# Kernel optimization log

Hardware: AMD Instinct MI355X
Metric: run time of the kernel (lower is better)

The kernel has to match this reference:

```python
import jax, jax.numpy as jnp
import numpy as np
from functools import partial

SAMPLE_RATE = 44100
CUTOFF_HZ = 20.0
# one-pole high-pass coefficient: y[i] = x[i] - x[i-1] + alpha * y[i-1]
ALPHA = float(np.exp(-2.0 * np.pi * CUTOFF_HZ / SAMPLE_RATE))


def setup_inputs() -> dict:
    key = jax.random.key(0)
    k1, k2, k3, k4 = jax.random.split(key, 4)
    B, N = 64, 262144
    return {
        "x": jax.random.normal(k1, (B, N), dtype=jnp.float32),
        "drive": jax.random.uniform(k2, (B, 1), dtype=jnp.float32),
        "bias": jax.random.uniform(k3, (B, 1), dtype=jnp.float32),
        "mix": jax.random.uniform(k4, (B, 1), dtype=jnp.float32),
        "type_idx": 0,
    }


def _waveshape(processed, type_idx):
    if type_idx == 0:
        return jnp.tanh(processed)
    elif type_idx == 1:
        return jnp.clip(processed, -1.0, 1.0)
    elif type_idx == 2:
        return jnp.abs(jnp.remainder(processed + 1.0, 4.0) - 2.0) - 1.0
    elif type_idx == 3:
        return jnp.sin(processed * (np.pi / 2))
    else:
        return processed / (1.0 + jnp.abs(processed))


def _high_pass_filter(x):
    # x: [B, N]; sequential first-order IIR over the time axis via lax.scan
    B = x.shape[0]
    zeros = jnp.zeros((B,), dtype=x.dtype)

    def step(carry, xt):
        last_x, last_y = carry
        yt = xt - last_x + ALPHA * last_y
        return (xt, yt), yt

    _, yT = jax.lax.scan(step, (zeros, zeros), x.T)  # yT: [N, B]
    return yT.T


def reference(x, drive, bias, mix, type_idx):
    drive_gain = jnp.power(10.0, drive * 2.4)
    dc_offset = bias * 2.0 - 1.0
    processed = (x + dc_offset) * drive_gain
    distorted = _waveshape(processed, type_idx)
    distorted = _high_pass_filter(distorted)
    return (1.0 - mix) * x + mix * distorted
```

## Files before the change

kernel.cpp:

```cpp
#include <hip/hip_runtime.h>
#include <math.h>

#define TPB 1024
#define WAVES (TPB / 64)
#define PER_WAVE 1024
#define BLK (WAVES * PER_WAVE)
#define HALO 2048
#define CSZ (BLK - HALO)

typedef float v4f __attribute__((ext_vector_type(4)));

__device__ __forceinline__ float shape(float xs, int ty, float g, float dc,
                                       float c1, float c0) {
    if (ty == 0) {
        float e2 = __builtin_amdgcn_exp2f(fmaf(xs, c1, c0));
        return fmaf(-2.0f, __builtin_amdgcn_rcpf(e2 + 1.0f), 1.0f);
    }
    float p = (xs + dc) * g;
    if (ty == 1) {
        return fminf(fmaxf(p, -1.0f), 1.0f);
    } else if (ty == 2) {
        float r = p + 1.0f;
        float rem = r - 4.0f * floorf(r * 0.25f);
        return fabsf(rem - 2.0f) - 1.0f;
    } else if (ty == 3) {
        return __sinf(p * 1.5707963267948966f);
    } else {
        return p / (1.0f + fabsf(p));
    }
}

__global__ void __launch_bounds__(TPB, 8)
dist_kernel(const float* __restrict__ x,
            const float* __restrict__ drive,
            const float* __restrict__ bias,
            const float* __restrict__ mix,
            const int* __restrict__ type_idx,
            float* __restrict__ out,
            int N, float alpha, float beta)
{
    const int row  = blockIdx.y;
    const int tid  = threadIdx.x;
    const int lane = tid & 63;
    const int wv   = tid >> 6;
    const int ty   = *type_idx;

    const float g  = exp2f(drive[row] * 7.972672880099267f);
    const float dc = bias[row] * 2.0f - 1.0f;
    const float mm = mix[row];
    const float om = 1.0f - mm;
    const float c1 = g * 2.8853900817779268f;
    const float c0 = dc * c1;

    const long long rowBase = (long long)row * (long long)N;
    const float* __restrict__ xr = x + rowBase;
    float* __restrict__ outr = out + rowBase;

    const int outStart = (int)blockIdx.x * CSZ;
    const int wbase = outStart - HALO + wv * PER_WAVE;

    v4f d4[4];
    v4f mx4[4];
    #pragma unroll
    for (int k = 0; k < 4; ++k) {
        const int j = wbase + k * 256 + lane * 4;
        if (j >= 0 && j + 4 <= N) {
            v4f xv = *reinterpret_cast<const v4f*>(xr + j);
            mx4[k].x = om * xv.x; d4[k].x = shape(xv.x, ty, g, dc, c1, c0);
            mx4[k].y = om * xv.y; d4[k].y = shape(xv.y, ty, g, dc, c1, c0);
            mx4[k].z = om * xv.z; d4[k].z = shape(xv.z, ty, g, dc, c1, c0);
            mx4[k].w = om * xv.w; d4[k].w = shape(xv.w, ty, g, dc, c1, c0);
        } else {
            float xs; bool in;
            in = (j+0 >= 0) && (j+0 < N); xs = in ? xr[j+0] : 0.0f; mx4[k].x = om * xs; d4[k].x = in ? shape(xs, ty, g, dc, c1, c0) : 0.0f;
            in = (j+1 >= 0) && (j+1 < N); xs = in ? xr[j+1] : 0.0f; mx4[k].y = om * xs; d4[k].y = in ? shape(xs, ty, g, dc, c1, c0) : 0.0f;
            in = (j+2 >= 0) && (j+2 < N); xs = in ? xr[j+2] : 0.0f; mx4[k].z = om * xs; d4[k].z = in ? shape(xs, ty, g, dc, c1, c0) : 0.0f;
            in = (j+3 >= 0) && (j+3 < N); xs = in ? xr[j+3] : 0.0f; mx4[k].w = om * xs; d4[k].w = in ? shape(xs, ty, g, dc, c1, c0) : 0.0f;
        }
    }

    const float a2 = alpha * alpha;
    const float a4 = a2 * a2;
    float iv[4];
    #pragma unroll
    for (int k = 0; k < 4; ++k) {
        float acc = d4[k].x;
        acc = fmaf(alpha, acc, d4[k].y);
        acc = fmaf(alpha, acc, d4[k].z);
        acc = fmaf(alpha, acc, d4[k].w);
        iv[k] = acc;
    }

    float a256;
    #pragma unroll
    for (int k = 0; k < 4; ++k) {
        float v = iv[k];
        float m = a4;
        #pragma unroll
        for (int off = 1; off < 64; off <<= 1) {
            float up = __shfl_up(v, off, 64);
            if (lane >= off) v = fmaf(m, up, v);
            m *= m;
        }
        iv[k] = v;
        a256 = m;
    }

    float T[4];
    T[0] = __shfl(iv[0], 63, 64);
    T[1] = __shfl(iv[1], 63, 64);
    T[2] = __shfl(iv[2], 63, 64);
    T[3] = __shfl(iv[3], 63, 64);
    const float Twave = fmaf(a256, fmaf(a256, fmaf(a256, T[0], T[1]), T[2]), T[3]);
    const float a1024 = (a256 * a256) * (a256 * a256);

    __shared__ float wtot[WAVES];
    if (lane == 0) wtot[wv] = Twave;
    __syncthreads();
    float P = 0.0f;
    for (int w = 0; w < wv; ++w) P = fmaf(a1024, P, wtot[w]);

    float apl = 1.0f, b = a4;
    #pragma unroll
    for (int i = 0; i < 6; ++i) { if ((lane >> i) & 1) apl *= b; b *= b; }

    float S  = 0.0f;
    float aK = 1.0f;
    #pragma unroll
    for (int k = 0; k < 4; ++k) {
        const int j = wbase + k * 256 + lane * 4;
        const float Ck = fmaf(aK, P, S);
        float ex = __shfl_up(iv[k], 1, 64);
        if (lane == 0) ex = 0.0f;
        const float zin = fmaf(apl, Ck, ex);

        if (j >= outStart && j < N) {
            float z = zin;
            v4f ov;
            float y;
            y = fmaf(-beta, z, d4[k].x); ov.x = fmaf(mm, y, mx4[k].x); z = fmaf(alpha, z, d4[k].x);
            y = fmaf(-beta, z, d4[k].y); ov.y = fmaf(mm, y, mx4[k].y); z = fmaf(alpha, z, d4[k].y);
            y = fmaf(-beta, z, d4[k].z); ov.z = fmaf(mm, y, mx4[k].z); z = fmaf(alpha, z, d4[k].z);
            y = fmaf(-beta, z, d4[k].w); ov.w = fmaf(mm, y, mx4[k].w);
            if (j + 4 <= N) {
                __builtin_nontemporal_store(ov, reinterpret_cast<v4f*>(outr + j));
            } else {
                if (j + 0 < N) outr[j + 0] = ov.x;
                if (j + 1 < N) outr[j + 1] = ov.y;
                if (j + 2 < N) outr[j + 2] = ov.z;
                if (j + 3 < N) outr[j + 3] = ov.w;
            }
        }
        S  = fmaf(a256, S, T[k]);
        aK *= a256;
    }
}

extern "C" void kernel_launch(void* const* d_in, const int* in_sizes, int n_in,
                              void* d_out, int out_size, void* d_ws, size_t ws_size,
                              hipStream_t stream) {
    const float* x     = (const float*)d_in[0];
    const float* drive = (const float*)d_in[1];
    const float* bias  = (const float*)d_in[2];
    const float* mixp  = (const float*)d_in[3];
    const int*   tyi   = (const int*)d_in[4];
    float* out = (float*)d_out;

    const int B = in_sizes[1];
    const int N = in_sizes[0] / B;

    const double alpha_d = exp(-2.0 * M_PI * 20.0 / 44100.0);
    const float alpha = (float)alpha_d;
    const float beta  = (float)(1.0 - alpha_d);

    const int nChunks = (N + CSZ - 1) / CSZ;
    dim3 grid(nChunks, B);
    dist_kernel<<<grid, TPB, 0, stream>>>(x, drive, bias, mixp, tyi, out, N, alpha, beta);
}
```

Baseline: 128.8 us.

## Loop persistent blocks over chunks with carried IIR state and DPP scans

Each block now walks several consecutive chunks of a row, carrying the IIR state across chunks instead of recomputing a large halo per chunk; only one halo segment per block is computed. The intra-wave scan uses DPP row operations and readlane instead of shuffles, and the next chunk's input is prefetched while the current one is processed. This reduces redundant halo loads and compute, but shrinks the grid to few blocks per row, which lowers parallelism and memory-level concurrency.

```diff
diff --git a/kernel.cpp b/kernel.cpp
--- a/kernel.cpp
+++ b/kernel.cpp
@@ -1,14 +1,37 @@
 #include <hip/hip_runtime.h>
 #include <math.h>
 
-#define TPB 1024
+#define TPB 512
 #define WAVES (TPB / 64)
 #define PER_WAVE 1024
-#define BLK (WAVES * PER_WAVE)
+#define CHUNK (WAVES * PER_WAVE)
+#define NB 8
 #define HALO 2048
-#define CSZ (BLK - HALO)
 
 typedef float v4f __attribute__((ext_vector_type(4)));
+
+template<int CTRL, int RM, int BM, bool BC>
+__device__ __forceinline__ float dppf(float v) {
+    return __int_as_float(__builtin_amdgcn_update_dpp(
+        0, __float_as_int(v), CTRL, RM, BM, BC));
+}
+
+__device__ __forceinline__ float readlane_f(float v, int l) {
+    return __int_as_float(__builtin_amdgcn_readlane(__float_as_int(v), l));
+}
+
+__device__ __forceinline__ float scan_iir(float v, float mo1, float mo2,
+                                          float mo4, float mo8,
+                                          float w1, float w2) {
+    float b;
+    b = dppf<0x111, 0xF, 0xF, true >(v); v = fmaf(mo1, b, v);
+    b = dppf<0x112, 0xF, 0xF, true >(v); v = fmaf(mo2, b, v);
+    b = dppf<0x114, 0xF, 0xF, true >(v); v = fmaf(mo4, b, v);
+    b = dppf<0x118, 0xF, 0xF, true >(v); v = fmaf(mo8, b, v);
+    b = dppf<0x142, 0xA, 0xF, false>(v); v = fmaf(w1,  b, v);
+    b = dppf<0x143, 0xC, 0xF, false>(v); v = fmaf(w2,  b, v);
+    return v;
+}
 
 __device__ __forceinline__ float shape(float xs, int ty, float g, float dc,
                                        float c1, float c0) {
@@ -30,7 +53,23 @@
     }
 }
 
-__global__ void __launch_bounds__(TPB, 8)
+__device__ __forceinline__ void load_chunk(v4f xv[4], const float* __restrict__ xr,
+                                           int base, int N) {
+    #pragma unroll
+    for (int k = 0; k < 4; ++k) {
+        const int j = base + k * 256;
+        if (j + 4 <= N) {
+            xv[k] = *reinterpret_cast<const v4f*>(xr + j);
+        } else {
+            xv[k].x = (j + 0 < N) ? xr[j + 0] : 0.0f;
+            xv[k].y = (j + 1 < N) ? xr[j + 1] : 0.0f;
+            xv[k].z = (j + 2 < N) ? xr[j + 2] : 0.0f;
+            xv[k].w = (j + 3 < N) ? xr[j + 3] : 0.0f;
+        }
+    }
+}
+
+__global__ void __launch_bounds__(TPB, 4)
 dist_kernel(const float* __restrict__ x,
             const float* __restrict__ drive,
             const float* __restrict__ bias,
@@ -40,10 +79,18 @@
             int N, float alpha, float beta)
 {
     const int row  = blockIdx.y;
+    const int bx   = blockIdx.x;
     const int tid  = threadIdx.x;
     const int lane = tid & 63;
     const int wv   = tid >> 6;
     const int ty   = *type_idx;
+
+    const int nChunks = (N + CHUNK - 1) / CHUNK;
+    const int cpb = (nChunks + NB - 1) / NB;
+    const int cFirst = bx * cpb;
+    if (cFirst >= nChunks) return;
+    const int cLast = min(cFirst + cpb, nChunks);
+    const int spanStart = cFirst * CHUNK;
 
     const float g  = exp2f(drive[row] * 7.972672880099267f);
     const float dc = bias[row] * 2.0f - 1.0f;
@@ -56,92 +103,104 @@
     const float* __restrict__ xr = x + rowBase;
     float* __restrict__ outr = out + rowBase;
 
-    const int outStart = (int)blockIdx.x * CSZ;
-    const int wbase = outStart - HALO + wv * PER_WAVE;
-
-    v4f d4[4];
-    v4f mx4[4];
-    #pragma unroll
-    for (int k = 0; k < 4; ++k) {
-        const int j = wbase + k * 256 + lane * 4;
-        if (j >= 0 && j + 4 <= N) {
-            v4f xv = *reinterpret_cast<const v4f*>(xr + j);
-            mx4[k].x = om * xv.x; d4[k].x = shape(xv.x, ty, g, dc, c1, c0);
-            mx4[k].y = om * xv.y; d4[k].y = shape(xv.y, ty, g, dc, c1, c0);
-            mx4[k].z = om * xv.z; d4[k].z = shape(xv.z, ty, g, dc, c1, c0);
-            mx4[k].w = om * xv.w; d4[k].w = shape(xv.w, ty, g, dc, c1, c0);
-        } else {
-            float xs; bool in;
-            in = (j+0 >= 0) && (j+0 < N); xs = in ? xr[j+0] : 0.0f; mx4[k].x = om * xs; d4[k].x = in ? shape(xs, ty, g, dc, c1, c0) : 0.0f;
-            in = (j+1 >= 0) && (j+1 < N); xs = in ? xr[j+1] : 0.0f; mx4[k].y = om * xs; d4[k].y = in ? shape(xs, ty, g, dc, c1, c0) : 0.0f;
-            in = (j+2 >= 0) && (j+2 < N); xs = in ? xr[j+2] : 0.0f; mx4[k].z = om * xs; d4[k].z = in ? shape(xs, ty, g, dc, c1, c0) : 0.0f;
-            in = (j+3 >= 0) && (j+3 < N); xs = in ? xr[j+3] : 0.0f; mx4[k].w = om * xs; d4[k].w = in ? shape(xs, ty, g, dc, c1, c0) : 0.0f;
-        }
-    }
-
-    const float a2 = alpha * alpha;
-    const float a4 = a2 * a2;
-    float iv[4];
-    #pragma unroll
-    for (int k = 0; k < 4; ++k) {
-        float acc = d4[k].x;
-        acc = fmaf(alpha, acc, d4[k].y);
-        acc = fmaf(alpha, acc, d4[k].z);
-        acc = fmaf(alpha, acc, d4[k].w);
-        iv[k] = acc;
-    }
-
-    float a256;
-    #pragma unroll
-    for (int k = 0; k < 4; ++k) {
-        float v = iv[k];
-        float m = a4;
-        #pragma unroll
-        for (int off = 1; off < 64; off <<= 1) {
-            float up = __shfl_up(v, off, 64);
-            if (lane >= off) v = fmaf(m, up, v);
-            m *= m;
-        }
-        iv[k] = v;
-        a256 = m;
-    }
-
-    float T[4];
-    T[0] = __shfl(iv[0], 63, 64);
-    T[1] = __shfl(iv[1], 63, 64);
-    T[2] = __shfl(iv[2], 63, 64);
-    T[3] = __shfl(iv[3], 63, 64);
-    const float Twave = fmaf(a256, fmaf(a256, fmaf(a256, T[0], T[1]), T[2]), T[3]);
-    const float a1024 = (a256 * a256) * (a256 * a256);
-
-    __shared__ float wtot[WAVES];
-    if (lane == 0) wtot[wv] = Twave;
+    const float A2 = alpha * alpha;
+    const float A4 = A2 * A2;
+    const float A8 = A4 * A4;
+    const float A16 = A8 * A8;
+    const float A32 = A16 * A16;
+    const float A64 = A32 * A32;
+    const float A128 = A64 * A64;
+    const float A256 = A128 * A128;
+    const float A512 = A256 * A256;
+    const float A1024 = A512 * A512;
+    const float invA4 = 1.0f / A4;
+
+    float p15 = 1.0f;
+    {
+        float b = A4; const int n = lane & 15;
+        #pragma unroll
+        for (int i = 0; i < 4; ++i) { if ((n >> i) & 1) p15 *= b; b *= b; }
+    }
+    const float p31 = (lane & 16) ? p15 * A64  : p15;
+    const float apl = (lane & 32) ? p31 * A128 : p31;
+    const float w1 = A4 * p15;
+    const float w2 = A4 * p31;
+
+    __shared__ float wtot[2][WAVES];
+    const int wvOff = wv * PER_WAVE + lane * 4;
+
+    v4f xc[4];
+    load_chunk(xc, xr, spanStart + wvOff, N);
+
+    float carry = 0.0f;
+    if (bx > 0) {
+        const int j = spanStart - HALO + wv * 256 + lane * 4;
+        const v4f hx = *reinterpret_cast<const v4f*>(xr + j);
+        float r = shape(hx.x, ty, g, dc, c1, c0);
+        r = fmaf(alpha, r, shape(hx.y, ty, g, dc, c1, c0));
+        r = fmaf(alpha, r, shape(hx.z, ty, g, dc, c1, c0));
+        r = fmaf(alpha, r, shape(hx.w, ty, g, dc, c1, c0));
+        const float s = scan_iir(r, A4, A8, A16, A32, w1, w2);
+        if (lane == 63) wtot[1][wv] = s;
+    }
     __syncthreads();
-    float P = 0.0f;
-    for (int w = 0; w < wv; ++w) P = fmaf(a1024, P, wtot[w]);
-
-    float apl = 1.0f, b = a4;
-    #pragma unroll
-    for (int i = 0; i < 6; ++i) { if ((lane >> i) & 1) apl *= b; b *= b; }
-
-    float S  = 0.0f;
-    float aK = 1.0f;
-    #pragma unroll
-    for (int k = 0; k < 4; ++k) {
-        const int j = wbase + k * 256 + lane * 4;
-        const float Ck = fmaf(aK, P, S);
-        float ex = __shfl_up(iv[k], 1, 64);
-        if (lane == 0) ex = 0.0f;
-        const float zin = fmaf(apl, Ck, ex);
-
-        if (j >= outStart && j < N) {
-            float z = zin;
-            v4f ov;
-            float y;
-            y = fmaf(-beta, z, d4[k].x); ov.x = fmaf(mm, y, mx4[k].x); z = fmaf(alpha, z, d4[k].x);
-            y = fmaf(-beta, z, d4[k].y); ov.y = fmaf(mm, y, mx4[k].y); z = fmaf(alpha, z, d4[k].y);
-            y = fmaf(-beta, z, d4[k].z); ov.z = fmaf(mm, y, mx4[k].z); z = fmaf(alpha, z, d4[k].z);
-            y = fmaf(-beta, z, d4[k].w); ov.w = fmaf(mm, y, mx4[k].w);
+    if (bx > 0) {
+        #pragma unroll
+        for (int w = 0; w < WAVES; ++w) carry = fmaf(A256, carry, wtot[1][w]);
+    }
+
+    int par = 0;
+    for (int c = cFirst; c < cLast; ++c, par ^= 1) {
+        const int cb = c * CHUNK;
+        const bool more = (c + 1 < cLast);
+        v4f xn[4];
+        if (more) load_chunk(xn, xr, cb + CHUNK + wvOff, N);
+
+        v4f d4[4];
+        #pragma unroll
+        for (int k = 0; k < 4; ++k) {
+            d4[k].x = shape(xc[k].x, ty, g, dc, c1, c0);
+            d4[k].y = shape(xc[k].y, ty, g, dc, c1, c0);
+            d4[k].z = shape(xc[k].z, ty, g, dc, c1, c0);
+            d4[k].w = shape(xc[k].w, ty, g, dc, c1, c0);
+        }
+
+        float rv[4], iv[4];
+        #pragma unroll
+        for (int k = 0; k < 4; ++k) {
+            float acc = d4[k].x;
+            acc = fmaf(alpha, acc, d4[k].y);
+            acc = fmaf(alpha, acc, d4[k].z);
+            acc = fmaf(alpha, acc, d4[k].w);
+            rv[k] = acc;
+            iv[k] = scan_iir(acc, A4, A8, A16, A32, w1, w2);
+        }
+
+        float Tk[4];
+        #pragma unroll
+        for (int k = 0; k < 4; ++k) Tk[k] = readlane_f(iv[k], 63);
+        const float Twave =
+            fmaf(A256, fmaf(A256, fmaf(A256, Tk[0], Tk[1]), Tk[2]), Tk[3]);
+        if (lane == 0) wtot[par][wv] = Twave;
+        __syncthreads();
+
+        float P = carry;
+        for (int w = 0; w < wv; ++w) P = fmaf(A1024, P, wtot[par][w]);
+        #pragma unroll
+        for (int w = 0; w < WAVES; ++w) carry = fmaf(A1024, carry, wtot[par][w]);
+
+        float S = 0.0f, aK = 1.0f;
+        #pragma unroll
+        for (int k = 0; k < 4; ++k) {
+            const int j = cb + wvOff + k * 256;
+            const float Ck = fmaf(aK, P, S);
+            const float ex = (iv[k] - rv[k]) * invA4;
+            float z = fmaf(apl, Ck, ex);
+            v4f ov; float y;
+            y = fmaf(-beta, z, d4[k].x); ov.x = fmaf(mm, y, om * xc[k].x); z = fmaf(alpha, z, d4[k].x);
+            y = fmaf(-beta, z, d4[k].y); ov.y = fmaf(mm, y, om * xc[k].y); z = fmaf(alpha, z, d4[k].y);
+            y = fmaf(-beta, z, d4[k].z); ov.z = fmaf(mm, y, om * xc[k].z); z = fmaf(alpha, z, d4[k].z);
+            y = fmaf(-beta, z, d4[k].w); ov.w = fmaf(mm, y, om * xc[k].w);
             if (j + 4 <= N) {
                 __builtin_nontemporal_store(ov, reinterpret_cast<v4f*>(outr + j));
             } else {
@@ -150,9 +209,14 @@
                 if (j + 2 < N) outr[j + 2] = ov.z;
                 if (j + 3 < N) outr[j + 3] = ov.w;
             }
-        }
-        S  = fmaf(a256, S, T[k]);
-        aK *= a256;
+            S = fmaf(A256, S, Tk[k]);
+            aK *= A256;
+        }
+
+        if (more) {
+            #pragma unroll
+            for (int k = 0; k < 4; ++k) xc[k] = xn[k];
+        }
     }
 }
 
@@ -173,7 +237,6 @@
     const float alpha = (float)alpha_d;
     const float beta  = (float)(1.0 - alpha_d);
 
-    const int nChunks = (N + CSZ - 1) / CSZ;
-    dim3 grid(nChunks, B);
+    dim3 grid(NB, B);
     dist_kernel<<<grid, TPB, 0, stream>>>(x, drive, bias, mixp, tyi, out, N, alpha, beta);
 }
```

Result: faster. 117.0 us (-9.2%).
